# Optimization experiments

Measured on AMD Instinct MI355X. Metric: run time of the kernel, lower is better.

The kernel has to match this reference:

```python
import jax, jax.numpy as jnp
import numpy as np

EPS = 1e-12  # tf.nn.l2_normalize epsilon used inside keras CosineSimilarity


def _cos(a, b):
    # keras CosineSimilarity returns -cos; callers negate explicitly.
    an = a / jnp.sqrt(jnp.maximum(jnp.sum(a * a, axis=-1, keepdims=True), EPS))
    bn = b / jnp.sqrt(jnp.maximum(jnp.sum(b * b, axis=-1, keepdims=True), EPS))
    return jnp.sum(an * bn, axis=-1)


def setup_inputs() -> dict:
    key = jax.random.key(0)
    B, S, D, H, N = 1024, 200, 128, 128, 64
    ks = jax.random.split(key, 8)
    X_series = jax.random.normal(ks[0], (B, S, D), jnp.float32)
    pos_series = jax.random.normal(ks[1], (S, D), jnp.float32)
    X_item = jax.random.normal(ks[2], (B, D), jnp.float32)
    origin = jax.random.normal(ks[3], (B, N, D), jnp.float32)  # X_negative
    # contiguous-prefix validity mask (module assumes valid positions form a prefix)
    lengths = jax.random.randint(ks[4], (B,), 1, S + 1)
    valid_mask = jnp.arange(S)[None, :] < lengths[:, None]
    # learned params (GlorotUniform-scale init)
    Wp = jax.random.normal(ks[5], (D, H), jnp.float32) * 0.08
    We = jax.random.normal(ks[6], (D, H), jnp.float32) * 0.08
    z = jax.random.normal(ks[7], (H,), jnp.float32) * 0.1
    return {"X_series": X_series, "pos_series": pos_series, "X_item": X_item,
            "valid_mask": valid_mask, "origin": origin, "Wp": Wp, "We": We, "z": z}


def reference(X_series, pos_series, X_item, valid_mask, origin, Wp, We, z):
    B, S, D = X_series.shape
    # additive tanh attention: z . tanh(X_series @ We + pos_series @ Wp)
    hidden = jnp.tanh(jnp.einsum('bsd,dh->bsh', X_series, We) + (pos_series @ Wp)[None])
    scores = jnp.einsum('bsh,h->bs', hidden, z)
    scores = jnp.where(valid_mask, scores, -jnp.inf)
    attn = jax.nn.softmax(scores, axis=-1)                      # [B,S]
    attentioned = attn[:, :, None] * X_series                    # [B,S,D]
    attention_output = jnp.sum(attentioned, axis=1)              # [B,D]
    inner = jnp.sum(attention_output * X_item, axis=-1, keepdims=True)
    concated = jnp.concatenate([attention_output, inner], axis=1)  # [B,D+1]

    # ---- auxiliary loss ----
    last_idx = jnp.sum(valid_mask.astype(jnp.int32), axis=1) - 1
    last_vec = attentioned[jnp.arange(B), last_idx]              # gather_nd
    new_mask = (jnp.arange(S)[None, :] < last_idx[:, None]).astype(X_series.dtype)
    out_vec = jnp.sum(attentioned * new_mask[:, :, None], axis=1)  # [B,D]
    # keras CosineSimilarity = -cos_sim; then mapped to (x+1)/2 and used as logits
    pos_logits = (-_cos(last_vec, out_vec) + 1.0) / 2.0          # [B]
    neg_logits = (-_cos(origin, out_vec[:, None, :]) + 1.0) / 2.0  # [B,N]
    pos_loss = jax.nn.softplus(-pos_logits)  # sigmoid_xent labels=1
    neg_loss = jax.nn.softplus(neg_logits)   # sigmoid_xent labels=0
    # NB: TF reduces pos_loss over its only axis -> scalar, broadcast-added to [B]
    auxiliary_loss = jnp.sum(pos_loss) + jnp.sum(neg_loss, axis=-1)  # [B]
    return concated, auxiliary_loss
```

## Files before the change

kernel.cpp:

```cpp
#include <hip/hip_runtime.h>
#include <hip/hip_bf16.h>
#include <math.h>

#define B_ 1024
#define S_ 200
#define D_ 128
#define H_ 128
#define N_ 64

typedef __attribute__((ext_vector_type(8))) short short8;
typedef __attribute__((ext_vector_type(8))) __bf16 bf16x8;
typedef __attribute__((ext_vector_type(4))) float floatx4;

typedef __attribute__((address_space(1))) void gvoid_t;
typedef __attribute__((address_space(3))) void lvoid_t;

static __device__ __forceinline__ float bf2f(unsigned short u) {
    union { unsigned int i; float f; } v; v.i = ((unsigned int)u) << 16; return v.f;
}
static __device__ __forceinline__ unsigned short f2bf(float f) {
    union { float f; unsigned int u; } v; v.f = f;
    unsigned int u = v.u;
    return (unsigned short)((u + 0x7FFFu + ((u >> 16) & 1u)) >> 16);
}
static __device__ __forceinline__ float ld1(const void* p, int isbf, size_t i) {
    return isbf ? bf2f(((const unsigned short*)p)[i]) : ((const float*)p)[i];
}
static __device__ __forceinline__ float fast_tanh(float x) {
    float t = __expf(2.0f * x);
    return 1.0f - 2.0f * __builtin_amdgcn_rcpf(t + 1.0f);
}
static __device__ __forceinline__ void gload_lds16(const void* g, void* l) {
    __builtin_amdgcn_global_load_lds((const gvoid_t*)g, (lvoid_t*)l, 16, 0, 0);
}

#define LBAR() { asm volatile("s_waitcnt lgkmcnt(0)" ::: "memory"); __builtin_amdgcn_s_barrier(); }

static __device__ __forceinline__ int detect_wave_256(const void* p) {
    int lane = threadIdx.x & 63;
    uint4 w = ((const uint4*)p)[lane];
    unsigned int ws[4] = {w.x, w.y, w.z, w.w};
    int pass = 0;
#pragma unroll
    for (int k = 0; k < 4; ++k) {
        unsigned int e = (ws[k] >> 7) & 0xFF;
        pass += (e == 0 || (e >= 96 && e <= 140)) ? 1 : 0;
    }
#pragma unroll
    for (int off = 32; off; off >>= 1) pass += __shfl_xor(pass, off, 64);
    return pass * 4 >= 256 * 3;
}
static __device__ __forceinline__ int detect_wave_64(const void* p) {
    int lane = threadIdx.x & 63;
    unsigned int w = ((const unsigned int*)p)[lane];
    unsigned int e = (w >> 7) & 0xFF;
    int pass = (e == 0 || (e >= 96 && e <= 140)) ? 1 : 0;
#pragma unroll
    for (int off = 32; off; off >>= 1) pass += __shfl_xor(pass, off, 64);
    return pass * 4 >= 64 * 3;
}
static __device__ __forceinline__ int detect_mask_u8(const void* p) {
    int lane = threadIdx.x & 63;
    uint4 w = ((const uint4*)p)[lane];
    unsigned int x = (w.x | w.y | w.z | w.w) & 0xFFFFFF00u;
    return (__ballot(x != 0) != 0ULL) ? 1 : 0;
}

__global__ __launch_bounds__(128) void prep_kernel(
    const void* __restrict__ We, const void* __restrict__ pos,
    const void* __restrict__ Wp,
    unsigned short* __restrict__ WeTf, unsigned short* __restrict__ pbLh,
    float* __restrict__ gsum, unsigned int* __restrict__ cnt)
{
    int blk = blockIdx.x, t = threadIdx.x;
    __shared__ unsigned short T[128][136];
    __shared__ float prow[D_];
    __shared__ int fl[2];
    if (blk == 0) {
        if (t == 0) { *gsum = 0.f; *cnt = 0u; }
        if (t < 64) { int f = detect_wave_256(We); if (t == 0) fl[0] = f; }
        __syncthreads();
        int fWe = fl[0];
        for (int c = t; c < 2048; c += 128) {
            int d = c >> 4, h8 = (c & 15) * 8;
            short8 v;
            if (fWe) {
                v = *(const short8*)((const unsigned short*)We + d * H_ + h8);
            } else {
                const float* p = (const float*)We + d * H_ + h8;
                float4 a = ((const float4*)p)[0], b = ((const float4*)p)[1];
                v[0] = (short)f2bf(a.x); v[1] = (short)f2bf(a.y);
                v[2] = (short)f2bf(a.z); v[3] = (short)f2bf(a.w);
                v[4] = (short)f2bf(b.x); v[5] = (short)f2bf(b.y);
                v[6] = (short)f2bf(b.z); v[7] = (short)f2bf(b.w);
            }
            *(short8*)(&T[d][h8]) = v;
        }
        __syncthreads();
        for (int i = t; i < 2048; i += 128) {
            int frag = i >> 6, ln = i & 63;
            int nt = frag >> 2, kks = frag & 3;
            int h = nt * 16 + (ln & 15);
            int dbase = kks * 32 + (ln >> 4) * 8;
            short8 v;
#pragma unroll
            for (int j = 0; j < 8; ++j) v[j] = (short)T[dbase + j][h];
            *(short8*)(WeTf + (size_t)i * 8) = v;
        }
        for (int i = t; i < 1024; i += 128) {
            int nt = i >> 7, j = i & 127;
            int q = 2 + (j >> 6), m = (j >> 2) & 15, r = j & 3;
            pbLh[(((96 + nt) * 64 + q * 16 + m) << 2) + r] = 0;
        }
    } else {
        if (t < 64)       { int f = detect_wave_256(pos); if (t == 0)  fl[0] = f; }
        else if (t < 128) { int f = detect_wave_256(Wp);  if (t == 64) fl[1] = f; }
        __syncthreads();
        int fPos = fl[0], fWp = fl[1];
        int s = blk - 1, h = t;
        prow[h] = ld1(pos, fPos, (size_t)s * D_ + h);
        __syncthreads();
        float acc = 0.f;
        if (fWp) {
            const unsigned short* W = (const unsigned short*)Wp;
            for (int d = 0; d < D_; ++d) acc = fmaf(prow[d], bf2f(W[d * H_ + h]), acc);
        } else {
            const float* W = (const float*)Wp;
            for (int d = 0; d < D_; ++d) acc = fmaf(prow[d], W[d * H_ + h], acc);
        }
        int mt = s >> 4, qr = s & 15;
        int idx = (((mt * 8 + (h >> 4)) * 64 + (qr >> 2) * 16 + (h & 15)) << 2) + (qr & 3);
        pbLh[idx] = f2bf(acc);
    }
}

__global__ __launch_bounds__(512, 4) void fused_kernel(
    const void* __restrict__ Xs, const void* __restrict__ Xitem,
    const void* __restrict__ maskv, const void* __restrict__ origin,
    const unsigned short* __restrict__ WeTf, const unsigned short* __restrict__ pbLh,
    const void* __restrict__ zv,
    float* __restrict__ neg_sum, float* __restrict__ gsum,
    unsigned int* __restrict__ cnt, float* __restrict__ out)
{
    int b = blockIdx.x, t = threadIdx.x;
    int wv = t >> 6, lane = t & 63;
    int quad = lane >> 4, mrow = lane & 15;

    __shared__ __align__(16) unsigned short Xsh[208 * D_];
    __shared__ __align__(16) float ubuf[4096];
    __shared__ float red4[512];
    __shared__ float attn[200];
    __shared__ float outv[D_];
    __shared__ float red[40];
    __shared__ int lastflag;

    float* sp = ubuf;

    int fXs = detect_wave_256(Xs);
    int fXi = detect_wave_256(Xitem);
    int fOr = detect_wave_256(origin);
    int fz  = detect_wave_64(zv);
    int fMk = detect_mask_u8(maskv);

    const unsigned short* Xg16 = (const unsigned short*)Xs + (size_t)b * S_ * D_;
    const float*          Xg32 = (const float*)Xs + (size_t)b * S_ * D_;

    int nt = wv;
    bf16x8 bfr[4];
#pragma unroll
    for (int kks = 0; kks < 4; ++kks)
        bfr[kks] = __builtin_bit_cast(bf16x8,
            *(const short8*)(WeTf + (size_t)((((nt << 2) + kks) << 6) + lane) * 8));
    float zl = ld1(zv, fz, nt * 16 + mrow);
    uint2 pbh[13];
#pragma unroll
    for (int m2 = 0; m2 < 13; ++m2)
        pbh[m2] = *(const uint2*)(pbLh + (size_t)(((m2 * 8 + nt) * 64 + lane) << 2));
    float xiv = (t < D_) ? ld1(Xitem, fXi, (size_t)b * D_ + t) : 0.f;

    if (fXs) {
#pragma unroll
        for (int mt = 0; mt < 13; ++mt) {
            int row = mt * 16 + wv * 2 + (lane >> 4);
            int srow = row < S_ ? row : 199;
            int c8 = (lane & 15) * 8;
            if (lane < 32)
                gload_lds16(Xg16 + (size_t)srow * D_ + (c8 ^ ((srow & 7) << 3)),
                            Xsh + (size_t)row * D_ + c8);
        }
    } else {
        for (int i = t; i < S_ * 16; i += 512) {
            int s = i >> 4, c8 = (i & 15) * 8;
            const float* p = Xg32 + (size_t)s * D_ + c8;
            float4 a = ((const float4*)p)[0], c = ((const float4*)p)[1];
            short8 v;
            v[0] = (short)f2bf(a.x); v[1] = (short)f2bf(a.y);
            v[2] = (short)f2bf(a.z); v[3] = (short)f2bf(a.w);
            v[4] = (short)f2bf(c.x); v[5] = (short)f2bf(c.y);
            v[6] = (short)f2bf(c.z); v[7] = (short)f2bf(c.w);
            *(short8*)(Xsh + s * D_ + (c8 ^ ((s & 7) << 3))) = v;
        }
        LBAR();
    }

#define PHASE(MT, REM)                                                               \
    asm volatile("s_waitcnt vmcnt(" #REM ")" ::: "memory");                          \
    __builtin_amdgcn_s_barrier();                                                    \
    {                                                                                \
        int r_ = (MT) * 16 + mrow;                                                   \
        int rbase_ = r_ * D_, rx_ = (r_ & 7) << 3;                                   \
        floatx4 acc_;                                                                \
        acc_[0] = bf2f((unsigned short)(pbh[MT].x & 0xffff));                        \
        acc_[1] = bf2f((unsigned short)(pbh[MT].x >> 16));                           \
        acc_[2] = bf2f((unsigned short)(pbh[MT].y & 0xffff));                        \
        acc_[3] = bf2f((unsigned short)(pbh[MT].y >> 16));                           \
        _Pragma("unroll")                                                            \
        for (int kks_ = 0; kks_ < 4; ++kks_) {                                       \
            bf16x8 af_ = __builtin_bit_cast(bf16x8,                                  \
                *(const short8*)(Xsh + rbase_ + ((kks_ * 32 + quad * 8) ^ rx_)));    \
            acc_ = __builtin_amdgcn_mfma_f32_16x16x32_bf16(af_, bfr[kks_], acc_, 0, 0, 0); \
        }                                                                            \
        _Pragma("unroll")                                                            \
        for (int rr_ = 0; rr_ < 4; ++rr_) {                                          \
            float v_ = fast_tanh(acc_[rr_]) * zl;                                    \
            v_ += __shfl_xor(v_, 1, 64);                                             \
            v_ += __shfl_xor(v_, 2, 64);                                             \
            v_ += __shfl_xor(v_, 4, 64);                                             \
            v_ += __shfl_xor(v_, 8, 64);                                             \
            int s_ = (MT) * 16 + quad * 4 + rr_;                                     \
            if (mrow == 0 && s_ < S_) sp[nt * 208 + s_] = v_;                        \
        }                                                                            \
    }

    PHASE(0, 12)  PHASE(1, 11)  PHASE(2, 10)  PHASE(3, 9)
    PHASE(4, 8)   PHASE(5, 7)   PHASE(6, 6)   PHASE(7, 5)
    PHASE(8, 4)   PHASE(9, 3)   PHASE(10, 2)  PHASE(11, 1)
    PHASE(12, 0)
#undef PHASE

    int len = 0;
#pragma unroll
    for (int k = 0; k < 4; ++k) {
        int s = lane + 64 * k;
        int nzv = 0;
        if (s < S_)
            nzv = fMk ? (((const unsigned char*)maskv)[(size_t)b * S_ + s] != 0)
                      : (((const int*)maskv)[(size_t)b * S_ + s] != 0);
        len += __popcll(__ballot(nzv));
    }
    int last = len - 1;
    int nn = t >> 3, part = t & 7;
    float o_f[16];
    if (fOr) {
        const unsigned short* p = (const unsigned short*)origin + ((size_t)b * N_ + nn) * D_ + part * 16;
#pragma unroll
        for (int j = 0; j < 2; ++j) {
            uint4 u = *(const uint4*)(p + j * 8);
            o_f[j*8+0] = bf2f((unsigned short)(u.x & 0xffff));
            o_f[j*8+1] = bf2f((unsigned short)(u.x >> 16));
            o_f[j*8+2] = bf2f((unsigned short)(u.y & 0xffff));
            o_f[j*8+3] = bf2f((unsigned short)(u.y >> 16));
            o_f[j*8+4] = bf2f((unsigned short)(u.z & 0xffff));
            o_f[j*8+5] = bf2f((unsigned short)(u.z >> 16));
            o_f[j*8+6] = bf2f((unsigned short)(u.w & 0xffff));
            o_f[j*8+7] = bf2f((unsigned short)(u.w >> 16));
        }
    } else {
        const float* p = (const float*)origin + ((size_t)b * N_ + nn) * D_ + part * 16;
#pragma unroll
        for (int j = 0; j < 4; ++j) {
            float4 v = *(const float4*)(p + j * 4);
            o_f[j*4+0] = v.x; o_f[j*4+1] = v.y; o_f[j*4+2] = v.z; o_f[j*4+3] = v.w;
        }
    }

    LBAR();

    if (wv == 0) {
        int sb = lane * 4;
        float s0 = 0.f, s1 = 0.f, s2 = 0.f, s3 = 0.f;
        if (lane < 50) {
#pragma unroll
            for (int n8 = 0; n8 < 8; ++n8) {
                float4 q = *(const float4*)(sp + n8 * 208 + sb);
                s0 += q.x; s1 += q.y; s2 += q.z; s3 += q.w;
            }
        }
        float m0 = (sb + 0 < len) ? s0 : -INFINITY;
        float m1 = (sb + 1 < len) ? s1 : -INFINITY;
        float m2 = (sb + 2 < len) ? s2 : -INFINITY;
        float m3 = (sb + 3 < len) ? s3 : -INFINITY;
        float m = fmaxf(fmaxf(m0, m1), fmaxf(m2, m3));
#pragma unroll
        for (int off = 32; off; off >>= 1) m = fmaxf(m, __shfl_xor(m, off, 64));
        float e0 = (sb + 0 < len) ? __expf(s0 - m) : 0.f;
        float e1 = (sb + 1 < len) ? __expf(s1 - m) : 0.f;
        float e2 = (sb + 2 < len) ? __expf(s2 - m) : 0.f;
        float e3 = (sb + 3 < len) ? __expf(s3 - m) : 0.f;
        float l = e0 + e1 + e2 + e3;
#pragma unroll
        for (int off = 32; off; off >>= 1) l += __shfl_xor(l, off, 64);
        float inv = 1.0f / l;
        if (lane < 50) {
            float4 av = {e0 * inv, e1 * inv, e2 * inv, e3 * inv};
            *(float4*)(attn + sb) = av;
        }
    }
    LBAR();

    {
        int spi = t >> 4;
        int d8 = (t & 15) * 8;
        float a0 = 0.f, a1 = 0.f, a2 = 0.f, a3 = 0.f;
        float a4 = 0.f, a5 = 0.f, a6 = 0.f, a7 = 0.f;
        if (fXs) {
            for (int s = spi; s < S_; s += 32) {
                float ww = attn[s];
                short8 v2 = *(const short8*)(Xsh + s * D_ + (d8 ^ ((s & 7) << 3)));
                a0 = fmaf(ww, bf2f((unsigned short)v2[0]), a0);
                a1 = fmaf(ww, bf2f((unsigned short)v2[1]), a1);
                a2 = fmaf(ww, bf2f((unsigned short)v2[2]), a2);
                a3 = fmaf(ww, bf2f((unsigned short)v2[3]), a3);
                a4 = fmaf(ww, bf2f((unsigned short)v2[4]), a4);
                a5 = fmaf(ww, bf2f((unsigned short)v2[5]), a5);
                a6 = fmaf(ww, bf2f((unsigned short)v2[6]), a6);
                a7 = fmaf(ww, bf2f((unsigned short)v2[7]), a7);
            }
        } else {
            for (int s = spi; s < S_; s += 32) {
                float ww = attn[s];
                const float* p = Xg32 + (size_t)s * D_ + d8;
                float4 u0 = ((const float4*)p)[0], u1 = ((const float4*)p)[1];
                a0 = fmaf(ww, u0.x, a0); a1 = fmaf(ww, u0.y, a1);
                a2 = fmaf(ww, u0.z, a2); a3 = fmaf(ww, u0.w, a3);
                a4 = fmaf(ww, u1.x, a4); a5 = fmaf(ww, u1.y, a5);
                a6 = fmaf(ww, u1.z, a6); a7 = fmaf(ww, u1.w, a7);
            }
        }
        float4 w0 = {a0, a1, a2, a3}, w1 = {a4, a5, a6, a7};
        *(float4*)(ubuf + spi * D_ + d8)     = w0;
        *(float4*)(ubuf + spi * D_ + d8 + 4) = w1;
    }
    LBAR();
    {
        int g = t >> 7, d = t & 127;
        float sgp = 0.f;
#pragma unroll
        for (int p = 0; p < 8; ++p) sgp += ubuf[(g * 8 + p) * D_ + d];
        red4[g * D_ + d] = sgp;
    }
    LBAR();

    if (t < D_) {
        float att = red4[t] + red4[D_ + t] + red4[2 * D_ + t] + red4[3 * D_ + t];
        float xl = fXs ? bf2f(Xsh[last * D_ + (t ^ ((last & 7) << 3))])
                       : Xg32[(size_t)last * D_ + t];
        float lv = attn[last] * xl;
        float ov = att - lv;
        outv[t] = ov;
        out[(size_t)b * (D_ + 1) + t] = att;
        float r0 = att * xiv;
        float r1 = lv * lv, r2 = lv * ov, r3 = ov * ov;
#pragma unroll
        for (int off = 32; off; off >>= 1) {
            r0 += __shfl_xor(r0, off, 64);
            r1 += __shfl_xor(r1, off, 64);
            r2 += __shfl_xor(r2, off, 64);
            r3 += __shfl_xor(r3, off, 64);
        }
        if (lane == 0) { red[wv] = r0; red[8 + wv] = r1; red[16 + wv] = r2; red[24 + wv] = r3; }
    }
    LBAR();
    float vv = red[24] + red[25];
    if (t == 0) {
        out[(size_t)b * (D_ + 1) + D_] = red[0] + red[1];
        float ll = red[8] + red[9], lo = red[16] + red[17];
        float cosv = lo / (sqrtf(fmaxf(ll, 1e-12f)) * sqrtf(fmaxf(vv, 1e-12f)));
        float pl = 0.5f * (1.f - cosv);
        atomicAdd(gsum, log1pf(expf(-pl)));
    }

    {
        float o_oo = 0.f, o_ov = 0.f;
#pragma unroll
        for (int j = 0; j < 16; ++j) {
            float wv_ = outv[part * 16 + j];
            o_oo = fmaf(o_f[j], o_f[j], o_oo);
            o_ov = fmaf(o_f[j], wv_, o_ov);
        }
        o_oo += __shfl_xor(o_oo, 1, 64); o_ov += __shfl_xor(o_ov, 1, 64);
        o_oo += __shfl_xor(o_oo, 2, 64); o_ov += __shfl_xor(o_ov, 2, 64);
        o_oo += __shfl_xor(o_oo, 4, 64); o_ov += __shfl_xor(o_ov, 4, 64);
        float ns = 0.f;
        if (part == 0) {
            float cosn = o_ov / (sqrtf(fmaxf(o_oo, 1e-12f)) * sqrtf(fmaxf(vv, 1e-12f)));
            float nl = 0.5f * (1.f - cosn);
            ns = log1pf(expf(nl));
        }
        ns += __shfl_xor(ns, 8, 64);
        ns += __shfl_xor(ns, 16, 64);
        ns += __shfl_xor(ns, 32, 64);
        if (lane == 0) red[32 + wv] = ns;
    }
    LBAR();
    if (t == 0) {
        float nsum = red[32] + red[33] + red[34] + red[35]
                   + red[36] + red[37] + red[38] + red[39];
        neg_sum[b] = nsum;
        __threadfence();
        unsigned int my = atomicAdd(cnt, 1u);
        lastflag = (my == B_ - 1) ? 1 : 0;
    }
    LBAR();
    if (lastflag) {
        __threadfence();
        float gs = *(volatile float*)gsum;
        for (int b2 = t; b2 < B_; b2 += 512)
            out[(size_t)B_ * (D_ + 1) + b2] = gs + neg_sum[b2];
    }
}

extern "C" void kernel_launch(void* const* d_in, const int* in_sizes, int n_in,
                              void* d_out, int out_size, void* d_ws, size_t ws_size,
                              hipStream_t stream) {
    const void* Xs     = d_in[0];
    const void* pos    = d_in[1];
    const void* Xitem  = d_in[2];
    const void* mask   = d_in[3];
    const void* origin = d_in[4];
    const void* Wp     = d_in[5];
    const void* We     = d_in[6];
    const void* zv     = d_in[7];

    unsigned short* WeTf = (unsigned short*)d_ws;
    unsigned short* pbLh = (unsigned short*)((char*)d_ws + 32768);
    float* neg_sum  = (float*)((char*)d_ws + 32768 + 53248);
    float* gsum     = neg_sum + B_;
    unsigned int* cnt = (unsigned int*)(gsum + 1);
    float* out = (float*)d_out;

    prep_kernel<<<201, 128, 0, stream>>>(We, pos, Wp, WeTf, pbLh, gsum, cnt);
    fused_kernel<<<B_, 512, 0, stream>>>(Xs, Xitem, mask, origin, WeTf, pbLh, zv,
                                         neg_sum, gsum, cnt, out);
}
```

Measured before the change: 270.5 us.

## Process four batches per block with double-buffered LDS prefetch of next batch

Each block now handles four consecutive batch rows and keeps two LDS buffers for X. While the current batch is computed, the next one is loaded asynchronously, and the per-batch weight fragments and positional bias are loaded once per block instead of once per batch. The grid shrinks to 256 blocks, launch bounds drop to 2 blocks per SM, and LDS use roughly doubles. This cuts occupancy and parallelism, and the finer-grained per-phase vmcnt waits are replaced by a single wait at the end of each iteration.

```diff
diff --git a/kernel.cpp b/kernel.cpp
--- a/kernel.cpp
+++ b/kernel.cpp
@@ -134,7 +134,7 @@
     }
 }
 
-__global__ __launch_bounds__(512, 4) void fused_kernel(
+__global__ __launch_bounds__(512, 2) void fused_kernel(
     const void* __restrict__ Xs, const void* __restrict__ Xitem,
     const void* __restrict__ maskv, const void* __restrict__ origin,
     const unsigned short* __restrict__ WeTf, const unsigned short* __restrict__ pbLh,
@@ -142,11 +142,11 @@
     float* __restrict__ neg_sum, float* __restrict__ gsum,
     unsigned int* __restrict__ cnt, float* __restrict__ out)
 {
-    int b = blockIdx.x, t = threadIdx.x;
+    int t = threadIdx.x;
     int wv = t >> 6, lane = t & 63;
     int quad = lane >> 4, mrow = lane & 15;
 
-    __shared__ __align__(16) unsigned short Xsh[208 * D_];
+    __shared__ __align__(16) unsigned short Xsh[2][S_ * D_];
     __shared__ __align__(16) float ubuf[4096];
     __shared__ float red4[512];
     __shared__ float attn[200];
@@ -162,9 +162,6 @@
     int fz  = detect_wave_64(zv);
     int fMk = detect_mask_u8(maskv);
 
-    const unsigned short* Xg16 = (const unsigned short*)Xs + (size_t)b * S_ * D_;
-    const float*          Xg32 = (const float*)Xs + (size_t)b * S_ * D_;
-
     int nt = wv;
     bf16x8 bfr[4];
 #pragma unroll
@@ -176,247 +173,256 @@
 #pragma unroll
     for (int m2 = 0; m2 < 13; ++m2)
         pbh[m2] = *(const uint2*)(pbLh + (size_t)(((m2 * 8 + nt) * 64 + lane) << 2));
-    float xiv = (t < D_) ? ld1(Xitem, fXi, (size_t)b * D_ + t) : 0.f;
-
-    if (fXs) {
+
+    auto stage = [&](int buf, int bb) {
+        unsigned short* dst = &Xsh[buf][0];
+        if (fXs) {
+            const unsigned short* g16 = (const unsigned short*)Xs + (size_t)bb * S_ * D_;
+            for (int i = t; i < S_ * 16; i += 512) {
+                int s = i >> 4, c8 = (i & 15) * 8;
+                gload_lds16(g16 + (size_t)s * D_ + (c8 ^ ((s & 7) << 3)), dst + (size_t)i * 8);
+            }
+        } else {
+            const float* g32 = (const float*)Xs + (size_t)bb * S_ * D_;
+            for (int i = t; i < S_ * 16; i += 512) {
+                int s = i >> 4, c8 = (i & 15) * 8;
+                const float* p = g32 + (size_t)s * D_ + c8;
+                float4 a = ((const float4*)p)[0], c = ((const float4*)p)[1];
+                short8 v;
+                v[0] = (short)f2bf(a.x); v[1] = (short)f2bf(a.y);
+                v[2] = (short)f2bf(a.z); v[3] = (short)f2bf(a.w);
+                v[4] = (short)f2bf(c.x); v[5] = (short)f2bf(c.y);
+                v[6] = (short)f2bf(c.z); v[7] = (short)f2bf(c.w);
+                *(short8*)(dst + s * D_ + (c8 ^ ((s & 7) << 3))) = v;
+            }
+        }
+    };
+
+    int b0 = blockIdx.x * 4;
+
+    stage(0, b0);
+    asm volatile("s_waitcnt vmcnt(0)" ::: "memory");
+    LBAR();
+
+#pragma unroll 1
+    for (int ib = 0; ib < 4; ++ib) {
+        int b = b0 + ib;
+        int buf = ib & 1;
+        const unsigned short* Xb = &Xsh[buf][0];
+        const float* Xg32 = (const float*)Xs + (size_t)b * S_ * D_;
+
+        int len = 0;
+#pragma unroll
+        for (int k = 0; k < 4; ++k) {
+            int s = lane + 64 * k;
+            int nzv = 0;
+            if (s < S_)
+                nzv = fMk ? (((const unsigned char*)maskv)[(size_t)b * S_ + s] != 0)
+                          : (((const int*)maskv)[(size_t)b * S_ + s] != 0);
+            len += __popcll(__ballot(nzv));
+        }
+        int last = len - 1;
+        float xiv = (t < D_) ? ld1(Xitem, fXi, (size_t)b * D_ + t) : 0.f;
+        int nn = t >> 3, part = t & 7;
+        float o_f[16];
+        if (fOr) {
+            const unsigned short* p = (const unsigned short*)origin + ((size_t)b * N_ + nn) * D_ + part * 16;
+#pragma unroll
+            for (int j = 0; j < 2; ++j) {
+                uint4 u = *(const uint4*)(p + j * 8);
+                o_f[j*8+0] = bf2f((unsigned short)(u.x & 0xffff));
+                o_f[j*8+1] = bf2f((unsigned short)(u.x >> 16));
+                o_f[j*8+2] = bf2f((unsigned short)(u.y & 0xffff));
+                o_f[j*8+3] = bf2f((unsigned short)(u.y >> 16));
+                o_f[j*8+4] = bf2f((unsigned short)(u.z & 0xffff));
+                o_f[j*8+5] = bf2f((unsigned short)(u.z >> 16));
+                o_f[j*8+6] = bf2f((unsigned short)(u.w & 0xffff));
+                o_f[j*8+7] = bf2f((unsigned short)(u.w >> 16));
+            }
+        } else {
+            const float* p = (const float*)origin + ((size_t)b * N_ + nn) * D_ + part * 16;
+#pragma unroll
+            for (int j = 0; j < 4; ++j) {
+                float4 v = *(const float4*)(p + j * 4);
+                o_f[j*4+0] = v.x; o_f[j*4+1] = v.y; o_f[j*4+2] = v.z; o_f[j*4+3] = v.w;
+            }
+        }
+
+        if (ib < 3) stage(buf ^ 1, b + 1);
+
 #pragma unroll
         for (int mt = 0; mt < 13; ++mt) {
-            int row = mt * 16 + wv * 2 + (lane >> 4);
-            int srow = row < S_ ? row : 199;
-            int c8 = (lane & 15) * 8;
-            if (lane < 32)
-                gload_lds16(Xg16 + (size_t)srow * D_ + (c8 ^ ((srow & 7) << 3)),
-                            Xsh + (size_t)row * D_ + c8);
-        }
-    } else {
-        for (int i = t; i < S_ * 16; i += 512) {
-            int s = i >> 4, c8 = (i & 15) * 8;
-            const float* p = Xg32 + (size_t)s * D_ + c8;
-            float4 a = ((const float4*)p)[0], c = ((const float4*)p)[1];
-            short8 v;
-            v[0] = (short)f2bf(a.x); v[1] = (short)f2bf(a.y);
-            v[2] = (short)f2bf(a.z); v[3] = (short)f2bf(a.w);
-            v[4] = (short)f2bf(c.x); v[5] = (short)f2bf(c.y);
-            v[6] = (short)f2bf(c.z); v[7] = (short)f2bf(c.w);
-            *(short8*)(Xsh + s * D_ + (c8 ^ ((s & 7) << 3))) = v;
-        }
-        LBAR();
-    }
-
-#define PHASE(MT, REM)                                                               \
-    asm volatile("s_waitcnt vmcnt(" #REM ")" ::: "memory");                          \
-    __builtin_amdgcn_s_barrier();                                                    \
-    {                                                                                \
-        int r_ = (MT) * 16 + mrow;                                                   \
-        int rbase_ = r_ * D_, rx_ = (r_ & 7) << 3;                                   \
-        floatx4 acc_;                                                                \
-        acc_[0] = bf2f((unsigned short)(pbh[MT].x & 0xffff));                        \
-        acc_[1] = bf2f((unsigned short)(pbh[MT].x >> 16));                           \
-        acc_[2] = bf2f((unsigned short)(pbh[MT].y & 0xffff));                        \
-        acc_[3] = bf2f((unsigned short)(pbh[MT].y >> 16));                           \
-        _Pragma("unroll")                                                            \
-        for (int kks_ = 0; kks_ < 4; ++kks_) {                                       \
-            bf16x8 af_ = __builtin_bit_cast(bf16x8,                                  \
-                *(const short8*)(Xsh + rbase_ + ((kks_ * 32 + quad * 8) ^ rx_)));    \
-            acc_ = __builtin_amdgcn_mfma_f32_16x16x32_bf16(af_, bfr[kks_], acc_, 0, 0, 0); \
-        }                                                                            \
-        _Pragma("unroll")                                                            \
-        for (int rr_ = 0; rr_ < 4; ++rr_) {                                          \
-            float v_ = fast_tanh(acc_[rr_]) * zl;                                    \
-            v_ += __shfl_xor(v_, 1, 64);                                             \
-            v_ += __shfl_xor(v_, 2, 64);                                             \
-            v_ += __shfl_xor(v_, 4, 64);                                             \
-            v_ += __shfl_xor(v_, 8, 64);                                             \
-            int s_ = (MT) * 16 + quad * 4 + rr_;                                     \
-            if (mrow == 0 && s_ < S_) sp[nt * 208 + s_] = v_;                        \
-        }                                                                            \
-    }
-
-    PHASE(0, 12)  PHASE(1, 11)  PHASE(2, 10)  PHASE(3, 9)
-    PHASE(4, 8)   PHASE(5, 7)   PHASE(6, 6)   PHASE(7, 5)
-    PHASE(8, 4)   PHASE(9, 3)   PHASE(10, 2)  PHASE(11, 1)
-    PHASE(12, 0)
-#undef PHASE
-
-    int len = 0;
-#pragma unroll
-    for (int k = 0; k < 4; ++k) {
-        int s = lane + 64 * k;
-        int nzv = 0;
-        if (s < S_)
-            nzv = fMk ? (((const unsigned char*)maskv)[(size_t)b * S_ + s] != 0)
-                      : (((const int*)maskv)[(size_t)b * S_ + s] != 0);
-        len += __popcll(__ballot(nzv));
-    }
-    int last = len - 1;
-    int nn = t >> 3, part = t & 7;
-    float o_f[16];
-    if (fOr) {
-        const unsigned short* p = (const unsigned short*)origin + ((size_t)b * N_ + nn) * D_ + part * 16;
-#pragma unroll
-        for (int j = 0; j < 2; ++j) {
-            uint4 u = *(const uint4*)(p + j * 8);
-            o_f[j*8+0] = bf2f((unsigned short)(u.x & 0xffff));
-            o_f[j*8+1] = bf2f((unsigned short)(u.x >> 16));
-            o_f[j*8+2] = bf2f((unsigned short)(u.y & 0xffff));
-            o_f[j*8+3] = bf2f((unsigned short)(u.y >> 16));
-            o_f[j*8+4] = bf2f((unsigned short)(u.z & 0xffff));
-            o_f[j*8+5] = bf2f((unsigned short)(u.z >> 16));
-            o_f[j*8+6] = bf2f((unsigned short)(u.w & 0xffff));
-            o_f[j*8+7] = bf2f((unsigned short)(u.w >> 16));
-        }
-    } else {
-        const float* p = (const float*)origin + ((size_t)b * N_ + nn) * D_ + part * 16;
-#pragma unroll
-        for (int j = 0; j < 4; ++j) {
-            float4 v = *(const float4*)(p + j * 4);
-            o_f[j*4+0] = v.x; o_f[j*4+1] = v.y; o_f[j*4+2] = v.z; o_f[j*4+3] = v.w;
-        }
-    }
-
-    LBAR();
-
-    if (wv == 0) {
-        int sb = lane * 4;
-        float s0 = 0.f, s1 = 0.f, s2 = 0.f, s3 = 0.f;
-        if (lane < 50) {
-#pragma unroll
-            for (int n8 = 0; n8 < 8; ++n8) {
-                float4 q = *(const float4*)(sp + n8 * 208 + sb);
-                s0 += q.x; s1 += q.y; s2 += q.z; s3 += q.w;
-            }
-        }
-        float m0 = (sb + 0 < len) ? s0 : -INFINITY;
-        float m1 = (sb + 1 < len) ? s1 : -INFINITY;
-        float m2 = (sb + 2 < len) ? s2 : -INFINITY;
-        float m3 = (sb + 3 < len) ? s3 : -INFINITY;
-        float m = fmaxf(fmaxf(m0, m1), fmaxf(m2, m3));
-#pragma unroll
-        for (int off = 32; off; off >>= 1) m = fmaxf(m, __shfl_xor(m, off, 64));
-        float e0 = (sb + 0 < len) ? __expf(s0 - m) : 0.f;
-        float e1 = (sb + 1 < len) ? __expf(s1 - m) : 0.f;
-        float e2 = (sb + 2 < len) ? __expf(s2 - m) : 0.f;
-        float e3 = (sb + 3 < len) ? __expf(s3 - m) : 0.f;
-        float l = e0 + e1 + e2 + e3;
-#pragma unroll
-        for (int off = 32; off; off >>= 1) l += __shfl_xor(l, off, 64);
-        float inv = 1.0f / l;
-        if (lane < 50) {
-            float4 av = {e0 * inv, e1 * inv, e2 * inv, e3 * inv};
-            *(float4*)(attn + sb) = av;
-        }
-    }
-    LBAR();
-
-    {
-        int spi = t >> 4;
-        int d8 = (t & 15) * 8;
-        float a0 = 0.f, a1 = 0.f, a2 = 0.f, a3 = 0.f;
-        float a4 = 0.f, a5 = 0.f, a6 = 0.f, a7 = 0.f;
-        if (fXs) {
-            for (int s = spi; s < S_; s += 32) {
-                float ww = attn[s];
-                short8 v2 = *(const short8*)(Xsh + s * D_ + (d8 ^ ((s & 7) << 3)));
-                a0 = fmaf(ww, bf2f((unsigned short)v2[0]), a0);
-                a1 = fmaf(ww, bf2f((unsigned short)v2[1]), a1);
-                a2 = fmaf(ww, bf2f((unsigned short)v2[2]), a2);
-                a3 = fmaf(ww, bf2f((unsigned short)v2[3]), a3);
-                a4 = fmaf(ww, bf2f((unsigned short)v2[4]), a4);
-                a5 = fmaf(ww, bf2f((unsigned short)v2[5]), a5);
-                a6 = fmaf(ww, bf2f((unsigned short)v2[6]), a6);
-                a7 = fmaf(ww, bf2f((unsigned short)v2[7]), a7);
-            }
-        } else {
-            for (int s = spi; s < S_; s += 32) {
-                float ww = attn[s];
-                const float* p = Xg32 + (size_t)s * D_ + d8;
-                float4 u0 = ((const float4*)p)[0], u1 = ((const float4*)p)[1];
-                a0 = fmaf(ww, u0.x, a0); a1 = fmaf(ww, u0.y, a1);
-                a2 = fmaf(ww, u0.z, a2); a3 = fmaf(ww, u0.w, a3);
-                a4 = fmaf(ww, u1.x, a4); a5 = fmaf(ww, u1.y, a5);
-                a6 = fmaf(ww, u1.z, a6); a7 = fmaf(ww, u1.w, a7);
-            }
-        }
-        float4 w0 = {a0, a1, a2, a3}, w1 = {a4, a5, a6, a7};
-        *(float4*)(ubuf + spi * D_ + d8)     = w0;
-        *(float4*)(ubuf + spi * D_ + d8 + 4) = w1;
-    }
-    LBAR();
-    {
-        int g = t >> 7, d = t & 127;
-        float sgp = 0.f;
-#pragma unroll
-        for (int p = 0; p < 8; ++p) sgp += ubuf[(g * 8 + p) * D_ + d];
-        red4[g * D_ + d] = sgp;
-    }
-    LBAR();
-
-    if (t < D_) {
-        float att = red4[t] + red4[D_ + t] + red4[2 * D_ + t] + red4[3 * D_ + t];
-        float xl = fXs ? bf2f(Xsh[last * D_ + (t ^ ((last & 7) << 3))])
-                       : Xg32[(size_t)last * D_ + t];
-        float lv = attn[last] * xl;
-        float ov = att - lv;
-        outv[t] = ov;
-        out[(size_t)b * (D_ + 1) + t] = att;
-        float r0 = att * xiv;
-        float r1 = lv * lv, r2 = lv * ov, r3 = ov * ov;
-#pragma unroll
-        for (int off = 32; off; off >>= 1) {
-            r0 += __shfl_xor(r0, off, 64);
-            r1 += __shfl_xor(r1, off, 64);
-            r2 += __shfl_xor(r2, off, 64);
-            r3 += __shfl_xor(r3, off, 64);
-        }
-        if (lane == 0) { red[wv] = r0; red[8 + wv] = r1; red[16 + wv] = r2; red[24 + wv] = r3; }
-    }
-    LBAR();
-    float vv = red[24] + red[25];
-    if (t == 0) {
-        out[(size_t)b * (D_ + 1) + D_] = red[0] + red[1];
-        float ll = red[8] + red[9], lo = red[16] + red[17];
-        float cosv = lo / (sqrtf(fmaxf(ll, 1e-12f)) * sqrtf(fmaxf(vv, 1e-12f)));
-        float pl = 0.5f * (1.f - cosv);
-        atomicAdd(gsum, log1pf(expf(-pl)));
-    }
-
-    {
-        float o_oo = 0.f, o_ov = 0.f;
-#pragma unroll
-        for (int j = 0; j < 16; ++j) {
-            float wv_ = outv[part * 16 + j];
-            o_oo = fmaf(o_f[j], o_f[j], o_oo);
-            o_ov = fmaf(o_f[j], wv_, o_ov);
-        }
-        o_oo += __shfl_xor(o_oo, 1, 64); o_ov += __shfl_xor(o_ov, 1, 64);
-        o_oo += __shfl_xor(o_oo, 2, 64); o_ov += __shfl_xor(o_ov, 2, 64);
-        o_oo += __shfl_xor(o_oo, 4, 64); o_ov += __shfl_xor(o_ov, 4, 64);
-        float ns = 0.f;
-        if (part == 0) {
-            float cosn = o_ov / (sqrtf(fmaxf(o_oo, 1e-12f)) * sqrtf(fmaxf(vv, 1e-12f)));
-            float nl = 0.5f * (1.f - cosn);
-            ns = log1pf(expf(nl));
-        }
-        ns += __shfl_xor(ns, 8, 64);
-        ns += __shfl_xor(ns, 16, 64);
-        ns += __shfl_xor(ns, 32, 64);
-        if (lane == 0) red[32 + wv] = ns;
-    }
-    LBAR();
-    if (t == 0) {
-        float nsum = red[32] + red[33] + red[34] + red[35]
-                   + red[36] + red[37] + red[38] + red[39];
-        neg_sum[b] = nsum;
-        __threadfence();
-        unsigned int my = atomicAdd(cnt, 1u);
-        lastflag = (my == B_ - 1) ? 1 : 0;
-    }
-    LBAR();
-    if (lastflag) {
-        __threadfence();
-        float gs = *(volatile float*)gsum;
-        for (int b2 = t; b2 < B_; b2 += 512)
-            out[(size_t)B_ * (D_ + 1) + b2] = gs + neg_sum[b2];
+            int r_ = mt * 16 + mrow; if (r_ > 199) r_ = 199;
+            int rbase_ = r_ * D_, rx_ = (r_ & 7) << 3;
+            floatx4 acc_;
+            acc_[0] = bf2f((unsigned short)(pbh[mt].x & 0xffff));
+            acc_[1] = bf2f((unsigned short)(pbh[mt].x >> 16));
+            acc_[2] = bf2f((unsigned short)(pbh[mt].y & 0xffff));
+            acc_[3] = bf2f((unsigned short)(pbh[mt].y >> 16));
+#pragma unroll
+            for (int kk = 0; kk < 4; ++kk) {
+                bf16x8 af = __builtin_bit_cast(bf16x8,
+                    *(const short8*)(Xb + rbase_ + ((kk * 32 + quad * 8) ^ rx_)));
+                acc_ = __builtin_amdgcn_mfma_f32_16x16x32_bf16(af, bfr[kk], acc_, 0, 0, 0);
+            }
+#pragma unroll
+            for (int rr = 0; rr < 4; ++rr) {
+                float v_ = fast_tanh(acc_[rr]) * zl;
+                v_ += __shfl_xor(v_, 1, 64);
+                v_ += __shfl_xor(v_, 2, 64);
+                v_ += __shfl_xor(v_, 4, 64);
+                v_ += __shfl_xor(v_, 8, 64);
+                int s_ = mt * 16 + quad * 4 + rr;
+                if (mrow == 0 && s_ < S_) sp[nt * 208 + s_] = v_;
+            }
+        }
+        LBAR();
+
+        if (wv == 0) {
+            int sb = lane * 4;
+            float s0 = 0.f, s1 = 0.f, s2 = 0.f, s3 = 0.f;
+            if (lane < 50) {
+#pragma unroll
+                for (int n8 = 0; n8 < 8; ++n8) {
+                    float4 q = *(const float4*)(sp + n8 * 208 + sb);
+                    s0 += q.x; s1 += q.y; s2 += q.z; s3 += q.w;
+                }
+            }
+            float m0 = (sb + 0 < len) ? s0 : -INFINITY;
+            float m1 = (sb + 1 < len) ? s1 : -INFINITY;
+            float m2 = (sb + 2 < len) ? s2 : -INFINITY;
+            float m3 = (sb + 3 < len) ? s3 : -INFINITY;
+            float m = fmaxf(fmaxf(m0, m1), fmaxf(m2, m3));
+#pragma unroll
+            for (int off = 32; off; off >>= 1) m = fmaxf(m, __shfl_xor(m, off, 64));
+            float e0 = (sb + 0 < len) ? __expf(s0 - m) : 0.f;
+            float e1 = (sb + 1 < len) ? __expf(s1 - m) : 0.f;
+            float e2 = (sb + 2 < len) ? __expf(s2 - m) : 0.f;
+            float e3 = (sb + 3 < len) ? __expf(s3 - m) : 0.f;
+            float l = e0 + e1 + e2 + e3;
+#pragma unroll
+            for (int off = 32; off; off >>= 1) l += __shfl_xor(l, off, 64);
+            float inv = 1.0f / l;
+            if (lane < 50) {
+                float4 av = {e0 * inv, e1 * inv, e2 * inv, e3 * inv};
+                *(float4*)(attn + sb) = av;
+            }
+        }
+        LBAR();
+
+        {
+            int spi = t >> 4;
+            int d8 = (t & 15) * 8;
+            float a0 = 0.f, a1 = 0.f, a2 = 0.f, a3 = 0.f;
+            float a4 = 0.f, a5 = 0.f, a6 = 0.f, a7 = 0.f;
+            if (fXs) {
+                for (int s = spi; s < S_; s += 32) {
+                    float ww = attn[s];
+                    short8 v2 = *(const short8*)(Xb + s * D_ + (d8 ^ ((s & 7) << 3)));
+                    a0 = fmaf(ww, bf2f((unsigned short)v2[0]), a0);
+                    a1 = fmaf(ww, bf2f((unsigned short)v2[1]), a1);
+                    a2 = fmaf(ww, bf2f((unsigned short)v2[2]), a2);
+                    a3 = fmaf(ww, bf2f((unsigned short)v2[3]), a3);
+                    a4 = fmaf(ww, bf2f((unsigned short)v2[4]), a4);
+                    a5 = fmaf(ww, bf2f((unsigned short)v2[5]), a5);
+                    a6 = fmaf(ww, bf2f((unsigned short)v2[6]), a6);
+                    a7 = fmaf(ww, bf2f((unsigned short)v2[7]), a7);
+                }
+            } else {
+                for (int s = spi; s < S_; s += 32) {
+                    float ww = attn[s];
+                    const float* p = Xg32 + (size_t)s * D_ + d8;
+                    float4 u0 = ((const float4*)p)[0], u1 = ((const float4*)p)[1];
+                    a0 = fmaf(ww, u0.x, a0); a1 = fmaf(ww, u0.y, a1);
+                    a2 = fmaf(ww, u0.z, a2); a3 = fmaf(ww, u0.w, a3);
+                    a4 = fmaf(ww, u1.x, a4); a5 = fmaf(ww, u1.y, a5);
+                    a6 = fmaf(ww, u1.z, a6); a7 = fmaf(ww, u1.w, a7);
+                }
+            }
+            float4 w0 = {a0, a1, a2, a3}, w1 = {a4, a5, a6, a7};
+            *(float4*)(ubuf + spi * D_ + d8)     = w0;
+            *(float4*)(ubuf + spi * D_ + d8 + 4) = w1;
+        }
+        LBAR();
+        {
+            int g = t >> 7, d = t & 127;
+            float sgp = 0.f;
+#pragma unroll
+            for (int p = 0; p < 8; ++p) sgp += ubuf[(g * 8 + p) * D_ + d];
+            red4[g * D_ + d] = sgp;
+        }
+        LBAR();
+
+        if (t < D_) {
+            float att = red4[t] + red4[D_ + t] + red4[2 * D_ + t] + red4[3 * D_ + t];
+            float xl = fXs ? bf2f(Xb[last * D_ + (t ^ ((last & 7) << 3))])
+                           : Xg32[(size_t)last * D_ + t];
+            float lv = attn[last] * xl;
+            float ov = att - lv;
+            outv[t] = ov;
+            out[(size_t)b * (D_ + 1) + t] = att;
+            float r0 = att * xiv;
+            float r1 = lv * lv, r2 = lv * ov, r3 = ov * ov;
+#pragma unroll
+            for (int off = 32; off; off >>= 1) {
+                r0 += __shfl_xor(r0, off, 64);
+                r1 += __shfl_xor(r1, off, 64);
+                r2 += __shfl_xor(r2, off, 64);
+                r3 += __shfl_xor(r3, off, 64);
+            }
+            if (lane == 0) { red[wv] = r0; red[8 + wv] = r1; red[16 + wv] = r2; red[24 + wv] = r3; }
+        }
+        LBAR();
+        float vv = red[24] + red[25];
+        if (t == 0) {
+            out[(size_t)b * (D_ + 1) + D_] = red[0] + red[1];
+            float ll = red[8] + red[9], lo = red[16] + red[17];
+            float cosv = lo / (sqrtf(fmaxf(ll, 1e-12f)) * sqrtf(fmaxf(vv, 1e-12f)));
+            float pl = 0.5f * (1.f - cosv);
+            atomicAdd(gsum, log1pf(expf(-pl)));
+        }
+
+        {
+            float o_oo = 0.f, o_ov = 0.f;
+#pragma unroll
+            for (int j = 0; j < 16; ++j) {
+                float wv_ = outv[part * 16 + j];
+                o_oo = fmaf(o_f[j], o_f[j], o_oo);
+                o_ov = fmaf(o_f[j], wv_, o_ov);
+            }
+            o_oo += __shfl_xor(o_oo, 1, 64); o_ov += __shfl_xor(o_ov, 1, 64);
+            o_oo += __shfl_xor(o_oo, 2, 64); o_ov += __shfl_xor(o_ov, 2, 64);
+            o_oo += __shfl_xor(o_oo, 4, 64); o_ov += __shfl_xor(o_ov, 4, 64);
+            float ns = 0.f;
+            if (part == 0) {
+                float cosn = o_ov / (sqrtf(fmaxf(o_oo, 1e-12f)) * sqrtf(fmaxf(vv, 1e-12f)));
+                float nl = 0.5f * (1.f - cosn);
+                ns = log1pf(expf(nl));
+            }
+            ns += __shfl_xor(ns, 8, 64);
+            ns += __shfl_xor(ns, 16, 64);
+            ns += __shfl_xor(ns, 32, 64);
+            if (lane == 0) red[32 + wv] = ns;
+        }
+        LBAR();
+        if (t == 0) {
+            float nsum = red[32] + red[33] + red[34] + red[35]
+                       + red[36] + red[37] + red[38] + red[39];
+            neg_sum[b] = nsum;
+            __threadfence();
+            unsigned int my = atomicAdd(cnt, 1u);
+            lastflag = (my == B_ - 1) ? 1 : 0;
+        }
+        LBAR();
+        if (lastflag) {
+            __threadfence();
+            float gs = *(volatile float*)gsum;
+            for (int b2 = t; b2 < B_; b2 += 512)
+                out[(size_t)B_ * (D_ + 1) + b2] = gs + neg_sum[b2];
+        }
+
+        asm volatile("s_waitcnt vmcnt(0)" ::: "memory");
+        __syncthreads();
     }
 }
 
@@ -440,6 +446,6 @@
     float* out = (float*)d_out;
 
     prep_kernel<<<201, 128, 0, stream>>>(We, pos, Wp, WeTf, pbLh, gsum, cnt);
-    fused_kernel<<<B_, 512, 0, stream>>>(Xs, Xitem, mask, origin, WeTf, pbLh, zv,
-                                         neg_sum, gsum, cnt, out);
-}
+    fused_kernel<<<B_ / 4, 512, 0, stream>>>(Xs, Xitem, mask, origin, WeTf, pbLh, zv,
+                                             neg_sum, gsum, cnt, out);
+}
```

After: 290.5 us. +7.4%, slower.
